# Kernel tuning notes

Hardware: AMD Instinct MI355X
Metric: run time of the kernel (lower is better)

The kernel has to match this reference:

```python
import jax, jax.numpy as jnp
import numpy as np

OVERFLOW_MARGIN = 1e-08
N, BBN_DIM, CBN_DIM = 8192, 32, 512


def setup_inputs() -> dict:
    key = jax.random.key(0)
    k1, k2, k3 = jax.random.split(key, 3)
    bbn = jax.random.uniform(k1, (N, BBN_DIM), dtype=jnp.float32)
    cbn = jax.random.normal(k2, (N, CBN_DIM), dtype=jnp.float32)
    # Dense(cbn_dim) params: glorot-ish init
    W = jax.random.normal(k3, (CBN_DIM, CBN_DIM), dtype=jnp.float32) / np.sqrt(CBN_DIM)
    b = jnp.zeros((CBN_DIM,), dtype=jnp.float32)
    return {"bbn": bbn, "cbn": cbn, "W": W, "b": b}


def reference(bbn, cbn, W, b):
    # --- build_adjacency_hamming(bbn): soft hamming-similarity adjacency [N,N] ---
    code_length = jnp.asarray(bbn.shape[1], dtype=bbn.dtype)
    m1 = bbn - 1.0
    c1 = bbn @ m1.T          # [N,N]
    c2 = m1 @ bbn.T          # [N,N]
    normalized_dist = jnp.abs(c1 + c2) / code_length
    adj = jnp.power(1.0 - normalized_dist, 1.4)

    # --- graph laplacian: D^{-1/2} A D^{-1/2} (broadcast form of eye*d_inv_sqrt matmuls) ---
    d = jnp.sum(adj, axis=1)                      # row sums == adj @ ones
    d_inv_sqrt = jnp.power(d + OVERFLOW_MARGIN, -0.5)
    laplacian = d_inv_sqrt[:, None] * adj * d_inv_sqrt[None, :]

    # --- GCN spectral conv: L @ Dense(cbn), then sigmoid ---
    fc_sc = cbn @ W + b                           # [N, cbn_dim]
    conv_sc = laplacian @ fc_sc                   # [N, cbn_dim]
    return jax.nn.sigmoid(conv_sc)
```

## Files before the change

### kernel.cpp

```cpp
#include <hip/hip_runtime.h>

#define NROWS 8192
#define BBND  32
#define CBND  512
#define JQ    4096
#define NR    64
#define ABUFB 8192

typedef unsigned short u16;
typedef unsigned int   u32;
typedef __bf16 bf16x8 __attribute__((ext_vector_type(8)));
typedef float  f32x4  __attribute__((ext_vector_type(4)));
typedef float  f32x16 __attribute__((ext_vector_type(16)));
typedef u32    u32x4  __attribute__((ext_vector_type(4)));
typedef u32    u32x2  __attribute__((ext_vector_type(2)));

#define ZERO4  (f32x4){0.f,0.f,0.f,0.f}
#define ZERO16 (f32x16){0.f,0.f,0.f,0.f,0.f,0.f,0.f,0.f,0.f,0.f,0.f,0.f,0.f,0.f,0.f,0.f}

#define BAR asm volatile("s_waitcnt lgkmcnt(0)\n\ts_barrier" ::: "memory")

static __device__ inline u16 f2bf(float f) {
    unsigned u = __builtin_bit_cast(unsigned, f);
    unsigned r = (u + 0x7FFFu + ((u >> 16) & 1u)) >> 16;
    return (u16)r;
}

static __device__ inline float pow14(float base) {
    return __builtin_amdgcn_exp2f(1.4f * __builtin_amdgcn_logf(base));
}

static __device__ inline float adj_eval(float dot, float sij) {
    float x = fabsf(2.f * dot - sij);
    float base = fmaxf(1.f - x * (1.f / 32.f), 0.f);
    return pow14(base);
}

static __device__ inline float sigmoidf_fast(float v) {
    float e = __builtin_amdgcn_exp2f(-1.44269504f * v);
    return 1.f / (1.f + e);
}

static __device__ inline u32 cvtpk(float a, float b) {
    u32 r;
    asm("v_cvt_pk_bf16_f32 %0, %1, %2" : "=v"(r) : "v"(a), "v"(b));
    return r;
}

static __device__ inline f32x4 MFMA16(bf16x8 a, bf16x8 b, f32x4 c) {
    return __builtin_amdgcn_mfma_f32_16x16x32_bf16(a, b, c, 0, 0, 0);
}
static __device__ inline f32x16 MFMA32(bf16x8 a, bf16x8 b, f32x16 c) {
    return __builtin_amdgcn_mfma_f32_32x32x16_bf16(a, b, c, 0, 0, 0);
}

__global__ __launch_bounds__(256) void k_prep_rows(const float* __restrict__ bbn,
                                                   float* __restrict__ s,
                                                   u16* __restrict__ bbn_bf) {
    int i = blockIdx.x * 256 + threadIdx.x;
    if (i >= NROWS) return;
    const f32x4* row = reinterpret_cast<const f32x4*>(bbn + i * BBND);
    float sum = 0.f;
    u16* dst = bbn_bf + i * BBND;
#pragma unroll
    for (int q = 0; q < 8; ++q) {
        f32x4 v = row[q];
#pragma unroll
        for (int e = 0; e < 4; ++e) {
            sum += v[e];
            dst[q * 4 + e] = f2bf(v[e]);
        }
    }
    s[i] = sum;
}

__global__ __launch_bounds__(256) void k_prep_wt(const float* __restrict__ W,
                                                 u16* __restrict__ WT) {
    int idx = blockIdx.x * 256 + threadIdx.x;
    int c = idx >> 9, k = idx & 511;
    WT[idx] = f2bf(W[k * CBND + c]);
}

__global__ __launch_bounds__(1024) void k_deg(const u16* __restrict__ bbn_bf,
                                              const float* __restrict__ s,
                                              float* __restrict__ dinv) {
    __shared__ float part[16][16];
    int ibase = blockIdx.x * 16;
    int tid = threadIdx.x;
    int w = tid >> 6, l = tid & 63, lg = l >> 4, lr = l & 15;

    bf16x8 afrag = *reinterpret_cast<const bf16x8*>(bbn_bf + (ibase + lr) * BBND + lg * 8);
    float si[4];
#pragma unroll
    for (int r = 0; r < 4; ++r) si[r] = s[ibase + lg * 4 + r];

    float dacc[4] = {0.f, 0.f, 0.f, 0.f};
    int j0 = w * (NROWS / 16);
    bf16x8 nbf = *reinterpret_cast<const bf16x8*>(bbn_bf + (j0 + lr) * BBND + lg * 8);
    float nsj = s[j0 + lr];
    for (int jt = 0; jt < NROWS / 16; jt += 16) {
        bf16x8 bfrag = nbf;
        float sj = nsj;
        if (jt + 16 < NROWS / 16) {
            int jn = j0 + jt + 16;
            nbf = *reinterpret_cast<const bf16x8*>(bbn_bf + (jn + lr) * BBND + lg * 8);
            nsj = s[jn + lr];
        }
        f32x4 dot = MFMA16(afrag, bfrag, ZERO4);
#pragma unroll
        for (int r = 0; r < 4; ++r) dacc[r] += adj_eval(dot[r], si[r] + sj);
    }
#pragma unroll
    for (int off = 1; off < 16; off <<= 1)
#pragma unroll
        for (int r = 0; r < 4; ++r) dacc[r] += __shfl_xor(dacc[r], off, 64);

    if (lr == 0) {
#pragma unroll
        for (int r = 0; r < 4; ++r) part[w][lg * 4 + r] = dacc[r];
    }
    __syncthreads();
    if (tid < 16) {
        float d = 0.f;
#pragma unroll
        for (int q = 0; q < 16; ++q) d += part[q][tid];
        dinv[ibase + tid] = rsqrtf(d + 1e-8f);
    }
}

__global__ __launch_bounds__(512) void k_fc(const float* __restrict__ cbn,
                                            const u16* __restrict__ WT,
                                            const float* __restrict__ bvec,
                                            const float* __restrict__ dinv,
                                            u16* __restrict__ g_blk) {
    __shared__ __align__(16) u16 Clds[64 * 512];
    int bx = blockIdx.x;
    int ch = bx & 1;
    int jcol = (bx >> 1) * 64;
    int tid = threadIdx.x;
    int w = tid >> 6, l = tid & 63, lg = l >> 4, lr = l & 15;
    int wq = w & 3, jh = w >> 2;

    char* Cl = (char*)&Clds[0];

#pragma unroll
    for (int p = 0; p < 8; ++p) {
        int gidx = p * 512 + tid;
        int row = gidx >> 6, sl = gidx & 63;
        const f32x4* src = reinterpret_cast<const f32x4*>(cbn + (jcol + row) * CBND + sl * 8);
        f32x4 v0 = src[0], v1 = src[1];
        bf16x8 bv;
#pragma unroll
        for (int e = 0; e < 4; ++e) { bv[e] = (__bf16)v0[e]; bv[e + 4] = (__bf16)v1[e]; }
        *reinterpret_cast<bf16x8*>(Cl + row * 1024 + ((sl ^ (row & 7)) << 4)) = bv;
    }
    __syncthreads();

    int r7 = lr & 7;
    for (int q = 0; q < 4; ++q) {
        int cb = ch * 4 + q;
        int crow = cb * 64 + wq * 16;
        f32x4 acc0 = ZERO4, acc1 = ZERO4;
        for (int k0 = 0; k0 < CBND; k0 += 32) {
            bf16x8 afrag = *reinterpret_cast<const bf16x8*>(WT + (crow + lr) * CBND + k0 + lg * 8);
            int slot = (k0 >> 3) + lg;
            int row0 = jh * 32 + lr;
            bf16x8 b0 = *reinterpret_cast<const bf16x8*>(Cl + row0 * 1024 + ((slot ^ r7) << 4));
            bf16x8 b1 = *reinterpret_cast<const bf16x8*>(Cl + (row0 + 16) * 1024 + ((slot ^ r7) << 4));
            acc0 = MFMA16(afrag, b0, acc0);
            acc1 = MFMA16(afrag, b1, acc1);
        }
#pragma unroll
        for (int f = 0; f < 2; ++f) {
            f32x4 af = f ? acc1 : acc0;
#pragma unroll
            for (int r = 0; r < 4; ++r) {
                int c = crow + lg * 4 + r;
                int j = jcol + jh * 32 + f * 16 + lr;
                float val = af[r] + bvec[c];
                g_blk[(((j >> 3) * 512 + c) << 3) + (j & 7)] = f2bf(val * dinv[j]);
            }
        }
    }
}


#define LOADB(T, R) { \
    const char* p = gB + (long)(T) * 65536; \
    R##0 = *reinterpret_cast<const u32x4*>(p); \
    R##1 = *reinterpret_cast<const u32x4*>(p + 16384); \
    R##2 = *reinterpret_cast<const u32x4*>(p + 32768); \
    R##3 = *reinterpret_cast<const u32x4*>(p + 49152); \
}

#define LOADG(ST) { \
    int jg = jbase + (ST) * 64 + jq8 * 16; \
    gJ = *reinterpret_cast<const bf16x8*>(bbn_bf + (jg + lr) * BBND + lg * 8); \
    gS = *reinterpret_cast<const f32x4*>(s + jg + lg * 4); \
}

#define GENP(WB) { \
    f32x4 dot = MFMA16(gJ, fragI, ZERO4); \
    u32 p0 = cvtpk(adj_eval(dot[0], si + gS[0]), adj_eval(dot[1], si + gS[1])); \
    u32 p1 = cvtpk(adj_eval(dot[2], si + gS[2]), adj_eval(dot[3], si + gS[3])); \
    *reinterpret_cast<u32x2*>(Ab + (WB) * ABUFB + gw) = (u32x2){p0, p1}; \
}

#define CONVP(RB, R) { \
    const char* Ar = Ab + (RB) * ABUFB; \
    bf16x8 t0l = *reinterpret_cast<const bf16x8*>(Ar + a0); \
    bf16x8 t0h = *reinterpret_cast<const bf16x8*>(Ar + a0 + 4096); \
    c00 = MFMA32(t0l, __builtin_bit_cast(bf16x8, R##0), c00); \
    c10 = MFMA32(t0h, __builtin_bit_cast(bf16x8, R##0), c10); \
    bf16x8 t1l = *reinterpret_cast<const bf16x8*>(Ar + a1); \
    bf16x8 t1h = *reinterpret_cast<const bf16x8*>(Ar + a1 + 4096); \
    c00 = MFMA32(t1l, __builtin_bit_cast(bf16x8, R##1), c00); \
    c10 = MFMA32(t1h, __builtin_bit_cast(bf16x8, R##1), c10); \
    bf16x8 t2l = *reinterpret_cast<const bf16x8*>(Ar + a2); \
    bf16x8 t2h = *reinterpret_cast<const bf16x8*>(Ar + a2 + 4096); \
    c00 = MFMA32(t2l, __builtin_bit_cast(bf16x8, R##2), c00); \
    c10 = MFMA32(t2h, __builtin_bit_cast(bf16x8, R##2), c10); \
    bf16x8 t3l = *reinterpret_cast<const bf16x8*>(Ar + a3); \
    bf16x8 t3h = *reinterpret_cast<const bf16x8*>(Ar + a3 + 4096); \
    c00 = MFMA32(t3l, __builtin_bit_cast(bf16x8, R##3), c00); \
    c10 = MFMA32(t3h, __builtin_bit_cast(bf16x8, R##3), c10); \
}

#define EPI(ACC, IH) { \
    _Pragma("unroll") \
    for (int reg = 0; reg < 16; ++reg) { \
        int rowD = (reg & 3) + 8 * (reg >> 2) + 4 * lh; \
        Pq[(long)(ibase + (IH) * 32 + rowD) * CBND + w * 32 + l31] = ACC[reg]; \
    } \
}

__global__ __launch_bounds__(1024, 4) void k_conv(const u16* __restrict__ bbn_bf,
                                                  const float* __restrict__ s,
                                                  const u16* __restrict__ g_blk,
                                                  float* __restrict__ P) {
    __shared__ __align__(16) u16 Alds[2][64 * 64];

    int bx = blockIdx.x;
    int jq = bx & 1;
    int it = bx >> 1;
    int ibase = it * 64;
    int jbase = jq * JQ;

    int tid = threadIdx.x;
    int w = tid >> 6, l = tid & 63;
    int lr = l & 15, lg = l >> 4, l31 = l & 31, lh = l >> 5;
    int iq = w & 3, jq8 = w >> 2;

    bf16x8 fragI = *reinterpret_cast<const bf16x8*>(bbn_bf + (ibase + iq * 16 + lr) * BBND + lg * 8);
    float si = s[ibase + iq * 16 + lr];

    char* Ab = (char*)&Alds[0][0];
    float* Pq = P + (long)jq * (NROWS * CBND);

    const char* gB = (const char*)g_blk + (long)jbase * 1024 + lh * 8192
                   + (w * 32 + l31) * 16;

    int r7 = l31 & 7;
    int abase = l31 * 128;
    int a0 = abase + (((0 + lh) ^ r7) << 4);
    int a1 = abase + (((2 + lh) ^ r7) << 4);
    int a2 = abase + (((4 + lh) ^ r7) << 4);
    int a3 = abase + (((6 + lh) ^ r7) << 4);

    int grow = iq * 16 + lr;
    int gw = grow * 128 + (((jq8 * 2 + (lg >> 1)) ^ (grow & 7)) << 4) + (lg & 1) * 8;

    f32x16 c00 = ZERO16, c10 = ZERO16;

    u32x4 rA0, rA1, rA2, rA3;
    u32x4 rB0, rB1, rB2, rB3;
    bf16x8 gJ;
    f32x4 gS;

    LOADG(0);
    GENP(0);
    LOADG(1);
    LOADB(0, rA);
    BAR;

    for (int st2 = 0; st2 < NR; st2 += 2) {
        LOADB(st2 + 1, rB);
        GENP(1);
        if (st2 + 2 < NR) LOADG(st2 + 2);
        CONVP(0, rA);
        BAR;
        int tn = (st2 + 2 < NR) ? st2 + 2 : NR - 1;
        LOADB(tn, rA);
        if (st2 + 2 < NR) {
            GENP(0);
            if (st2 + 3 < NR) LOADG(st2 + 3);
        }
        CONVP(1, rB);
        BAR;
    }

    EPI(c00, 0);
    EPI(c10, 1);
}

__global__ __launch_bounds__(256) void k_comb(const float* __restrict__ dinv,
                                              const float* __restrict__ P,
                                              float* __restrict__ out) {
    int idx = blockIdx.x * 256 + threadIdx.x;
    float di = dinv[idx >> 7];
    f32x4 a = *reinterpret_cast<const f32x4*>(P + (long)idx * 4);
    f32x4 b = *reinterpret_cast<const f32x4*>(P + (long)NROWS * CBND + (long)idx * 4);
    f32x4 v;
#pragma unroll
    for (int e = 0; e < 4; ++e) v[e] = sigmoidf_fast((a[e] + b[e]) * di);
    *reinterpret_cast<f32x4*>(out + (long)idx * 4) = v;
}

extern "C" void kernel_launch(void* const* d_in, const int* in_sizes, int n_in,
                              void* d_out, int out_size, void* d_ws, size_t ws_size,
                              hipStream_t stream) {
    const float* bbn = (const float*)d_in[0];
    const float* cbn = (const float*)d_in[1];
    const float* W   = (const float*)d_in[2];
    const float* b   = (const float*)d_in[3];
    float* out = (float*)d_out;

    char* ws = (char*)d_ws;
    float* s      = (float*)ws;  ws += NROWS * 4;
    float* dinv   = (float*)ws;  ws += NROWS * 4;
    u16* bbn_bf   = (u16*)ws;    ws += NROWS * BBND * 2;
    u16* WT       = (u16*)ws;    ws += CBND * CBND * 2;
    u16* g_blk    = (u16*)ws;    ws += (size_t)CBND * NROWS * 2;
    float* P      = (float*)ws;  ws += (size_t)2 * NROWS * CBND * 4;

    k_prep_rows<<<NROWS / 256, 256, 0, stream>>>(bbn, s, bbn_bf);
    k_prep_wt<<<(CBND * CBND) / 256, 256, 0, stream>>>(W, WT);
    k_deg<<<NROWS / 16, 1024, 0, stream>>>(bbn_bf, s, dinv);
    k_fc<<<(NROWS / 64) * 2, 512, 0, stream>>>(cbn, WT, b, dinv, g_blk);
    k_conv<<<(NROWS / 64) * 2, 1024, 0, stream>>>(bbn_bf, s, g_blk, P);
    k_comb<<<(NROWS * CBND / 4) / 256, 256, 0, stream>>>(dinv, P, out);
}
```

Baseline: 148.7 us.

## Fuse all six stages into one cooperative persistent kernel with grid syncs

Merges row prep, weight transpose, degree computation, the dense layer, the graph convolution and the sigmoid combine into a single kernel launched cooperatively with 256 blocks of 1024 threads. Stages are separated by grid-wide barriers, and one shared-memory buffer is reused across them. This targets the launch gaps and tail idle time between the six small kernels. The cost is that the early stages run with far fewer threads and a different work split, and every grid sync adds its own latency. The 64 KB of shared memory per block may also limit occupancy.

Result: slower. 265.8 us (+78.8%).

```diff
diff --git a/kernel.cpp b/kernel.cpp
--- a/kernel.cpp
+++ b/kernel.cpp
@@ -1,4 +1,7 @@
 #include <hip/hip_runtime.h>
+#include <hip/hip_cooperative_groups.h>
+
+namespace cg = cooperative_groups;
 
 #define NROWS 8192
 #define BBND  32
@@ -53,137 +56,6 @@
 static __device__ inline f32x16 MFMA32(bf16x8 a, bf16x8 b, f32x16 c) {
     return __builtin_amdgcn_mfma_f32_32x32x16_bf16(a, b, c, 0, 0, 0);
 }
-
-__global__ __launch_bounds__(256) void k_prep_rows(const float* __restrict__ bbn,
-                                                   float* __restrict__ s,
-                                                   u16* __restrict__ bbn_bf) {
-    int i = blockIdx.x * 256 + threadIdx.x;
-    if (i >= NROWS) return;
-    const f32x4* row = reinterpret_cast<const f32x4*>(bbn + i * BBND);
-    float sum = 0.f;
-    u16* dst = bbn_bf + i * BBND;
-#pragma unroll
-    for (int q = 0; q < 8; ++q) {
-        f32x4 v = row[q];
-#pragma unroll
-        for (int e = 0; e < 4; ++e) {
-            sum += v[e];
-            dst[q * 4 + e] = f2bf(v[e]);
-        }
-    }
-    s[i] = sum;
-}
-
-__global__ __launch_bounds__(256) void k_prep_wt(const float* __restrict__ W,
-                                                 u16* __restrict__ WT) {
-    int idx = blockIdx.x * 256 + threadIdx.x;
-    int c = idx >> 9, k = idx & 511;
-    WT[idx] = f2bf(W[k * CBND + c]);
-}
-
-__global__ __launch_bounds__(1024) void k_deg(const u16* __restrict__ bbn_bf,
-                                              const float* __restrict__ s,
-                                              float* __restrict__ dinv) {
-    __shared__ float part[16][16];
-    int ibase = blockIdx.x * 16;
-    int tid = threadIdx.x;
-    int w = tid >> 6, l = tid & 63, lg = l >> 4, lr = l & 15;
-
-    bf16x8 afrag = *reinterpret_cast<const bf16x8*>(bbn_bf + (ibase + lr) * BBND + lg * 8);
-    float si[4];
-#pragma unroll
-    for (int r = 0; r < 4; ++r) si[r] = s[ibase + lg * 4 + r];
-
-    float dacc[4] = {0.f, 0.f, 0.f, 0.f};
-    int j0 = w * (NROWS / 16);
-    bf16x8 nbf = *reinterpret_cast<const bf16x8*>(bbn_bf + (j0 + lr) * BBND + lg * 8);
-    float nsj = s[j0 + lr];
-    for (int jt = 0; jt < NROWS / 16; jt += 16) {
-        bf16x8 bfrag = nbf;
-        float sj = nsj;
-        if (jt + 16 < NROWS / 16) {
-            int jn = j0 + jt + 16;
-            nbf = *reinterpret_cast<const bf16x8*>(bbn_bf + (jn + lr) * BBND + lg * 8);
-            nsj = s[jn + lr];
-        }
-        f32x4 dot = MFMA16(afrag, bfrag, ZERO4);
-#pragma unroll
-        for (int r = 0; r < 4; ++r) dacc[r] += adj_eval(dot[r], si[r] + sj);
-    }
-#pragma unroll
-    for (int off = 1; off < 16; off <<= 1)
-#pragma unroll
-        for (int r = 0; r < 4; ++r) dacc[r] += __shfl_xor(dacc[r], off, 64);
-
-    if (lr == 0) {
-#pragma unroll
-        for (int r = 0; r < 4; ++r) part[w][lg * 4 + r] = dacc[r];
-    }
-    __syncthreads();
-    if (tid < 16) {
-        float d = 0.f;
-#pragma unroll
-        for (int q = 0; q < 16; ++q) d += part[q][tid];
-        dinv[ibase + tid] = rsqrtf(d + 1e-8f);
-    }
-}
-
-__global__ __launch_bounds__(512) void k_fc(const float* __restrict__ cbn,
-                                            const u16* __restrict__ WT,
-                                            const float* __restrict__ bvec,
-                                            const float* __restrict__ dinv,
-                                            u16* __restrict__ g_blk) {
-    __shared__ __align__(16) u16 Clds[64 * 512];
-    int bx = blockIdx.x;
-    int ch = bx & 1;
-    int jcol = (bx >> 1) * 64;
-    int tid = threadIdx.x;
-    int w = tid >> 6, l = tid & 63, lg = l >> 4, lr = l & 15;
-    int wq = w & 3, jh = w >> 2;
-
-    char* Cl = (char*)&Clds[0];
-
-#pragma unroll
-    for (int p = 0; p < 8; ++p) {
-        int gidx = p * 512 + tid;
-        int row = gidx >> 6, sl = gidx & 63;
-        const f32x4* src = reinterpret_cast<const f32x4*>(cbn + (jcol + row) * CBND + sl * 8);
-        f32x4 v0 = src[0], v1 = src[1];
-        bf16x8 bv;
-#pragma unroll
-        for (int e = 0; e < 4; ++e) { bv[e] = (__bf16)v0[e]; bv[e + 4] = (__bf16)v1[e]; }
-        *reinterpret_cast<bf16x8*>(Cl + row * 1024 + ((sl ^ (row & 7)) << 4)) = bv;
-    }
-    __syncthreads();
-
-    int r7 = lr & 7;
-    for (int q = 0; q < 4; ++q) {
-        int cb = ch * 4 + q;
-        int crow = cb * 64 + wq * 16;
-        f32x4 acc0 = ZERO4, acc1 = ZERO4;
-        for (int k0 = 0; k0 < CBND; k0 += 32) {
-            bf16x8 afrag = *reinterpret_cast<const bf16x8*>(WT + (crow + lr) * CBND + k0 + lg * 8);
-            int slot = (k0 >> 3) + lg;
-            int row0 = jh * 32 + lr;
-            bf16x8 b0 = *reinterpret_cast<const bf16x8*>(Cl + row0 * 1024 + ((slot ^ r7) << 4));
-            bf16x8 b1 = *reinterpret_cast<const bf16x8*>(Cl + (row0 + 16) * 1024 + ((slot ^ r7) << 4));
-            acc0 = MFMA16(afrag, b0, acc0);
-            acc1 = MFMA16(afrag, b1, acc1);
-        }
-#pragma unroll
-        for (int f = 0; f < 2; ++f) {
-            f32x4 af = f ? acc1 : acc0;
-#pragma unroll
-            for (int r = 0; r < 4; ++r) {
-                int c = crow + lg * 4 + r;
-                int j = jcol + jh * 32 + f * 16 + lr;
-                float val = af[r] + bvec[c];
-                g_blk[(((j >> 3) * 512 + c) << 3) + (j & 7)] = f2bf(val * dinv[j]);
-            }
-        }
-    }
-}
-
 
 #define LOADB(T, R) { \
     const char* p = gB + (long)(T) * 65536; \
@@ -234,86 +106,210 @@
     } \
 }
 
-__global__ __launch_bounds__(1024, 4) void k_conv(const u16* __restrict__ bbn_bf,
-                                                  const float* __restrict__ s,
-                                                  const u16* __restrict__ g_blk,
-                                                  float* __restrict__ P) {
-    __shared__ __align__(16) u16 Alds[2][64 * 64];
+__global__ __launch_bounds__(1024, 4) void k_fused(
+        const float* __restrict__ bbn, const float* __restrict__ cbn,
+        const float* __restrict__ W, const float* __restrict__ bvec,
+        float* __restrict__ out,
+        float* __restrict__ s, float* __restrict__ dinv,
+        u16* __restrict__ bbn_bf, u16* __restrict__ WT,
+        u16* __restrict__ g_blk, float* __restrict__ P) {
+    __shared__ __align__(16) char smem[65536];
+    __shared__ float part[2][8][16];
+
+    cg::grid_group gg = cg::this_grid();
 
     int bx = blockIdx.x;
-    int jq = bx & 1;
-    int it = bx >> 1;
-    int ibase = it * 64;
-    int jbase = jq * JQ;
-
     int tid = threadIdx.x;
     int w = tid >> 6, l = tid & 63;
     int lr = l & 15, lg = l >> 4, l31 = l & 31, lh = l >> 5;
-    int iq = w & 3, jq8 = w >> 2;
-
-    bf16x8 fragI = *reinterpret_cast<const bf16x8*>(bbn_bf + (ibase + iq * 16 + lr) * BBND + lg * 8);
-    float si = s[ibase + iq * 16 + lr];
-
-    char* Ab = (char*)&Alds[0][0];
-    float* Pq = P + (long)jq * (NROWS * CBND);
-
-    const char* gB = (const char*)g_blk + (long)jbase * 1024 + lh * 8192
-                   + (w * 32 + l31) * 16;
-
-    int r7 = l31 & 7;
-    int abase = l31 * 128;
-    int a0 = abase + (((0 + lh) ^ r7) << 4);
-    int a1 = abase + (((2 + lh) ^ r7) << 4);
-    int a2 = abase + (((4 + lh) ^ r7) << 4);
-    int a3 = abase + (((6 + lh) ^ r7) << 4);
-
-    int grow = iq * 16 + lr;
-    int gw = grow * 128 + (((jq8 * 2 + (lg >> 1)) ^ (grow & 7)) << 4) + (lg & 1) * 8;
-
-    f32x16 c00 = ZERO16, c10 = ZERO16;
-
-    u32x4 rA0, rA1, rA2, rA3;
-    u32x4 rB0, rB1, rB2, rB3;
-    bf16x8 gJ;
-    f32x4 gS;
-
-    LOADG(0);
-    GENP(0);
-    LOADG(1);
-    LOADB(0, rA);
-    BAR;
-
-    for (int st2 = 0; st2 < NR; st2 += 2) {
-        LOADB(st2 + 1, rB);
-        GENP(1);
-        if (st2 + 2 < NR) LOADG(st2 + 2);
-        CONVP(0, rA);
+
+    {
+        int idx = bx * 1024 + tid;
+        int c = idx >> 9, k = idx & 511;
+        WT[idx] = f2bf(W[k * CBND + c]);
+        if (idx < NROWS) {
+            const f32x4* row = reinterpret_cast<const f32x4*>(bbn + idx * BBND);
+            float sum = 0.f;
+            u16* dst = bbn_bf + idx * BBND;
+#pragma unroll
+            for (int q = 0; q < 8; ++q) {
+                f32x4 v = row[q];
+#pragma unroll
+                for (int e = 0; e < 4; ++e) {
+                    sum += v[e];
+                    dst[q * 4 + e] = f2bf(v[e]);
+                }
+            }
+            s[idx] = sum;
+        }
+    }
+    gg.sync();
+
+    {
+        int ibase = bx * 32;
+        int ig = w >> 3, jr = w & 7;
+        int ib = ibase + ig * 16;
+        bf16x8 afrag = *reinterpret_cast<const bf16x8*>(bbn_bf + (ib + lr) * BBND + lg * 8);
+        float si[4];
+#pragma unroll
+        for (int r = 0; r < 4; ++r) si[r] = s[ib + lg * 4 + r];
+
+        float dacc[4] = {0.f, 0.f, 0.f, 0.f};
+        int j0 = jr * 1024;
+        bf16x8 nbf = *reinterpret_cast<const bf16x8*>(bbn_bf + (j0 + lr) * BBND + lg * 8);
+        float nsj = s[j0 + lr];
+        for (int jt = 0; jt < 1024; jt += 16) {
+            bf16x8 bfrag = nbf;
+            float sj = nsj;
+            if (jt + 16 < 1024) {
+                int jn = j0 + jt + 16;
+                nbf = *reinterpret_cast<const bf16x8*>(bbn_bf + (jn + lr) * BBND + lg * 8);
+                nsj = s[jn + lr];
+            }
+            f32x4 dot = MFMA16(afrag, bfrag, ZERO4);
+#pragma unroll
+            for (int r = 0; r < 4; ++r) dacc[r] += adj_eval(dot[r], si[r] + sj);
+        }
+#pragma unroll
+        for (int off = 1; off < 16; off <<= 1)
+#pragma unroll
+            for (int r = 0; r < 4; ++r) dacc[r] += __shfl_xor(dacc[r], off, 64);
+
+        if (lr == 0) {
+#pragma unroll
+            for (int r = 0; r < 4; ++r) part[ig][jr][lg * 4 + r] = dacc[r];
+        }
+        __syncthreads();
+        if (tid < 32) {
+            int g2 = tid >> 4, rr = tid & 15;
+            float d = 0.f;
+#pragma unroll
+            for (int q = 0; q < 8; ++q) d += part[g2][q][rr];
+            dinv[ibase + g2 * 16 + rr] = rsqrtf(d + 1e-8f);
+        }
+    }
+    gg.sync();
+
+    {
+        char* Cl = smem;
+        int ch = bx & 1;
+        int jcol = (bx >> 1) * 64;
+#pragma unroll
+        for (int p = 0; p < 4; ++p) {
+            int gidx = p * 1024 + tid;
+            int row = gidx >> 6, sl = gidx & 63;
+            const f32x4* src = reinterpret_cast<const f32x4*>(cbn + (jcol + row) * CBND + sl * 8);
+            f32x4 v0 = src[0], v1 = src[1];
+            bf16x8 bv;
+#pragma unroll
+            for (int e = 0; e < 4; ++e) { bv[e] = (__bf16)v0[e]; bv[e + 4] = (__bf16)v1[e]; }
+            *reinterpret_cast<bf16x8*>(Cl + row * 1024 + ((sl ^ (row & 7)) << 4)) = bv;
+        }
+        __syncthreads();
+
+        int wq = w & 3, jh = (w >> 2) & 1, qh = w >> 3;
+        int r7 = lr & 7;
+#pragma unroll
+        for (int qq = 0; qq < 2; ++qq) {
+            int cb = ch * 4 + qh * 2 + qq;
+            int crow = cb * 64 + wq * 16;
+            f32x4 acc0 = ZERO4, acc1 = ZERO4;
+            for (int k0 = 0; k0 < CBND; k0 += 32) {
+                bf16x8 afrag = *reinterpret_cast<const bf16x8*>(WT + (crow + lr) * CBND + k0 + lg * 8);
+                int slot = (k0 >> 3) + lg;
+                int row0 = jh * 32 + lr;
+                bf16x8 b0 = *reinterpret_cast<const bf16x8*>(Cl + row0 * 1024 + ((slot ^ r7) << 4));
+                bf16x8 b1 = *reinterpret_cast<const bf16x8*>(Cl + (row0 + 16) * 1024 + ((slot ^ r7) << 4));
+                acc0 = MFMA16(afrag, b0, acc0);
+                acc1 = MFMA16(afrag, b1, acc1);
+            }
+#pragma unroll
+            for (int f = 0; f < 2; ++f) {
+                f32x4 af = f ? acc1 : acc0;
+#pragma unroll
+                for (int r = 0; r < 4; ++r) {
+                    int c = crow + lg * 4 + r;
+                    int j = jcol + jh * 32 + f * 16 + lr;
+                    float val = af[r] + bvec[c];
+                    g_blk[(((j >> 3) * 512 + c) << 3) + (j & 7)] = f2bf(val * dinv[j]);
+                }
+            }
+        }
+    }
+    gg.sync();
+
+    {
+        int jq = bx & 1;
+        int it = bx >> 1;
+        int ibase = it * 64;
+        int jbase = jq * JQ;
+        int iq = w & 3, jq8 = w >> 2;
+
+        bf16x8 fragI = *reinterpret_cast<const bf16x8*>(bbn_bf + (ibase + iq * 16 + lr) * BBND + lg * 8);
+        float si = s[ibase + iq * 16 + lr];
+
+        char* Ab = smem;
+        float* Pq = P + (long)jq * (NROWS * CBND);
+
+        const char* gB = (const char*)g_blk + (long)jbase * 1024 + lh * 8192
+                       + (w * 32 + l31) * 16;
+
+        int r7 = l31 & 7;
+        int abase = l31 * 128;
+        int a0 = abase + (((0 + lh) ^ r7) << 4);
+        int a1 = abase + (((2 + lh) ^ r7) << 4);
+        int a2 = abase + (((4 + lh) ^ r7) << 4);
+        int a3 = abase + (((6 + lh) ^ r7) << 4);
+
+        int grow = iq * 16 + lr;
+        int gw = grow * 128 + (((jq8 * 2 + (lg >> 1)) ^ (grow & 7)) << 4) + (lg & 1) * 8;
+
+        f32x16 c00 = ZERO16, c10 = ZERO16;
+        u32x4 rA0, rA1, rA2, rA3;
+        u32x4 rB0, rB1, rB2, rB3;
+        bf16x8 gJ;
+        f32x4 gS;
+
+        LOADG(0);
+        GENP(0);
+        LOADG(1);
+        LOADB(0, rA);
         BAR;
-        int tn = (st2 + 2 < NR) ? st2 + 2 : NR - 1;
-        LOADB(tn, rA);
-        if (st2 + 2 < NR) {
-            GENP(0);
-            if (st2 + 3 < NR) LOADG(st2 + 3);
-        }
-        CONVP(1, rB);
-        BAR;
-    }
-
-    EPI(c00, 0);
-    EPI(c10, 1);
-}
-
-__global__ __launch_bounds__(256) void k_comb(const float* __restrict__ dinv,
-                                              const float* __restrict__ P,
-                                              float* __restrict__ out) {
-    int idx = blockIdx.x * 256 + threadIdx.x;
-    float di = dinv[idx >> 7];
-    f32x4 a = *reinterpret_cast<const f32x4*>(P + (long)idx * 4);
-    f32x4 b = *reinterpret_cast<const f32x4*>(P + (long)NROWS * CBND + (long)idx * 4);
-    f32x4 v;
-#pragma unroll
-    for (int e = 0; e < 4; ++e) v[e] = sigmoidf_fast((a[e] + b[e]) * di);
-    *reinterpret_cast<f32x4*>(out + (long)idx * 4) = v;
+
+        for (int st2 = 0; st2 < NR; st2 += 2) {
+            LOADB(st2 + 1, rB);
+            GENP(1);
+            if (st2 + 2 < NR) LOADG(st2 + 2);
+            CONVP(0, rA);
+            BAR;
+            int tn = (st2 + 2 < NR) ? st2 + 2 : NR - 1;
+            LOADB(tn, rA);
+            if (st2 + 2 < NR) {
+                GENP(0);
+                if (st2 + 3 < NR) LOADG(st2 + 3);
+            }
+            CONVP(1, rB);
+            BAR;
+        }
+
+        EPI(c00, 0);
+        EPI(c10, 1);
+    }
+    gg.sync();
+
+    {
+#pragma unroll
+        for (int t = 0; t < 4; ++t) {
+            int idx = t * 262144 + bx * 1024 + tid;
+            float di = dinv[idx >> 7];
+            f32x4 a = *reinterpret_cast<const f32x4*>(P + (long)idx * 4);
+            f32x4 b = *reinterpret_cast<const f32x4*>(P + (long)NROWS * CBND + (long)idx * 4);
+            f32x4 v;
+#pragma unroll
+            for (int e = 0; e < 4; ++e) v[e] = sigmoidf_fast((a[e] + b[e]) * di);
+            *reinterpret_cast<f32x4*>(out + (long)idx * 4) = v;
+        }
+    }
 }
 
 extern "C" void kernel_launch(void* const* d_in, const int* in_sizes, int n_in,
@@ -333,10 +329,9 @@
     u16* g_blk    = (u16*)ws;    ws += (size_t)CBND * NROWS * 2;
     float* P      = (float*)ws;  ws += (size_t)2 * NROWS * CBND * 4;
 
-    k_prep_rows<<<NROWS / 256, 256, 0, stream>>>(bbn, s, bbn_bf);
-    k_prep_wt<<<(CBND * CBND) / 256, 256, 0, stream>>>(W, WT);
-    k_deg<<<NROWS / 16, 1024, 0, stream>>>(bbn_bf, s, dinv);
-    k_fc<<<(NROWS / 64) * 2, 512, 0, stream>>>(cbn, WT, b, dinv, g_blk);
-    k_conv<<<(NROWS / 64) * 2, 1024, 0, stream>>>(bbn_bf, s, g_blk, P);
-    k_comb<<<(NROWS * CBND / 4) / 256, 256, 0, stream>>>(dinv, P, out);
-}
+    void* kargs[] = {(void*)&bbn, (void*)&cbn, (void*)&W, (void*)&b, (void*)&out,
+                     (void*)&s, (void*)&dinv, (void*)&bbn_bf, (void*)&WT,
+                     (void*)&g_blk, (void*)&P};
+    hipLaunchCooperativeKernel(reinterpret_cast<const void*>(k_fused),
+                               dim3(256), dim3(1024), kargs, 0, stream);
+}
```

## Fuse prep kernels and fold final combine into conv via last-block flag

Applied to the files above, without the earlier changes.

Merges the two prep kernels into one launch that also zeroes a per-row-tile counter array. The separate combine kernel is removed: each conv block atomically increments a counter for its row tile, and the second block to finish sums both partial P halves, scales by dinv and applies the sigmoid. This removes two kernel launches and their gaps, and reads P while it is likely still in cache. In exchange it adds atomics and threadfences, and the tail of the conv kernel becomes uneven because only half the blocks run the epilogue.

Measured after the change: 290.6 us. +95.4%, slower.

```diff
diff --git a/kernel.cpp b/kernel.cpp
--- a/kernel.cpp
+++ b/kernel.cpp
@@ -54,31 +54,31 @@
     return __builtin_amdgcn_mfma_f32_32x32x16_bf16(a, b, c, 0, 0, 0);
 }
 
-__global__ __launch_bounds__(256) void k_prep_rows(const float* __restrict__ bbn,
-                                                   float* __restrict__ s,
-                                                   u16* __restrict__ bbn_bf) {
-    int i = blockIdx.x * 256 + threadIdx.x;
-    if (i >= NROWS) return;
-    const f32x4* row = reinterpret_cast<const f32x4*>(bbn + i * BBND);
-    float sum = 0.f;
-    u16* dst = bbn_bf + i * BBND;
-#pragma unroll
-    for (int q = 0; q < 8; ++q) {
-        f32x4 v = row[q];
-#pragma unroll
-        for (int e = 0; e < 4; ++e) {
-            sum += v[e];
-            dst[q * 4 + e] = f2bf(v[e]);
-        }
-    }
-    s[i] = sum;
-}
-
-__global__ __launch_bounds__(256) void k_prep_wt(const float* __restrict__ W,
-                                                 u16* __restrict__ WT) {
-    int idx = blockIdx.x * 256 + threadIdx.x;
+__global__ __launch_bounds__(512) void k_prep(const float* __restrict__ bbn,
+                                              const float* __restrict__ W,
+                                              float* __restrict__ s,
+                                              u16* __restrict__ bbn_bf,
+                                              u16* __restrict__ WT,
+                                              int* __restrict__ flags) {
+    int idx = blockIdx.x * 512 + threadIdx.x;
     int c = idx >> 9, k = idx & 511;
     WT[idx] = f2bf(W[k * CBND + c]);
+    if (idx < 128) flags[idx] = 0;
+    if (idx < NROWS) {
+        const f32x4* row = reinterpret_cast<const f32x4*>(bbn + idx * BBND);
+        float sum = 0.f;
+        u16* dst = bbn_bf + idx * BBND;
+#pragma unroll
+        for (int q = 0; q < 8; ++q) {
+            f32x4 v = row[q];
+#pragma unroll
+            for (int e = 0; e < 4; ++e) {
+                sum += v[e];
+                dst[q * 4 + e] = f2bf(v[e]);
+            }
+        }
+        s[idx] = sum;
+    }
 }
 
 __global__ __launch_bounds__(1024) void k_deg(const u16* __restrict__ bbn_bf,
@@ -236,9 +236,13 @@
 
 __global__ __launch_bounds__(1024, 4) void k_conv(const u16* __restrict__ bbn_bf,
                                                   const float* __restrict__ s,
+                                                  const float* __restrict__ dinv,
                                                   const u16* __restrict__ g_blk,
-                                                  float* __restrict__ P) {
+                                                  float* __restrict__ P,
+                                                  int* __restrict__ flags,
+                                                  float* __restrict__ out) {
     __shared__ __align__(16) u16 Alds[2][64 * 64];
+    __shared__ int s_old;
 
     int bx = blockIdx.x;
     int jq = bx & 1;
@@ -301,19 +305,27 @@
 
     EPI(c00, 0);
     EPI(c10, 1);
-}
-
-__global__ __launch_bounds__(256) void k_comb(const float* __restrict__ dinv,
-                                              const float* __restrict__ P,
-                                              float* __restrict__ out) {
-    int idx = blockIdx.x * 256 + threadIdx.x;
-    float di = dinv[idx >> 7];
-    f32x4 a = *reinterpret_cast<const f32x4*>(P + (long)idx * 4);
-    f32x4 b = *reinterpret_cast<const f32x4*>(P + (long)NROWS * CBND + (long)idx * 4);
-    f32x4 v;
-#pragma unroll
-    for (int e = 0; e < 4; ++e) v[e] = sigmoidf_fast((a[e] + b[e]) * di);
-    *reinterpret_cast<f32x4*>(out + (long)idx * 4) = v;
+
+    __syncthreads();
+    __threadfence();
+    if (tid == 0) s_old = atomicAdd(&flags[it], 1);
+    __syncthreads();
+    if (s_old == 1) {
+        __threadfence();
+#pragma unroll
+        for (int p = 0; p < 8; ++p) {
+            int idx = p * 1024 + tid;
+            int row = idx >> 7, c4 = idx & 127;
+            long off = (long)(ibase + row) * CBND + c4 * 4;
+            float di = dinv[ibase + row];
+            f32x4 a = *reinterpret_cast<const f32x4*>(P + off);
+            f32x4 b = *reinterpret_cast<const f32x4*>(P + (long)NROWS * CBND + off);
+            f32x4 v;
+#pragma unroll
+            for (int e = 0; e < 4; ++e) v[e] = sigmoidf_fast((a[e] + b[e]) * di);
+            *reinterpret_cast<f32x4*>(out + off) = v;
+        }
+    }
 }
 
 extern "C" void kernel_launch(void* const* d_in, const int* in_sizes, int n_in,
@@ -332,11 +344,10 @@
     u16* WT       = (u16*)ws;    ws += CBND * CBND * 2;
     u16* g_blk    = (u16*)ws;    ws += (size_t)CBND * NROWS * 2;
     float* P      = (float*)ws;  ws += (size_t)2 * NROWS * CBND * 4;
-
-    k_prep_rows<<<NROWS / 256, 256, 0, stream>>>(bbn, s, bbn_bf);
-    k_prep_wt<<<(CBND * CBND) / 256, 256, 0, stream>>>(W, WT);
+    int* flags    = (int*)ws;    ws += 128 * 4;
+
+    k_prep<<<512, 512, 0, stream>>>(bbn, W, s, bbn_bf, WT, flags);
     k_deg<<<NROWS / 16, 1024, 0, stream>>>(bbn_bf, s, dinv);
     k_fc<<<(NROWS / 64) * 2, 512, 0, stream>>>(cbn, WT, b, dinv, g_blk);
-    k_conv<<<(NROWS / 64) * 2, 1024, 0, stream>>>(bbn_bf, s, g_blk, P);
-    k_comb<<<(NROWS * CBND / 4) / 256, 256, 0, stream>>>(dinv, P, out);
-}
+    k_conv<<<(NROWS / 64) * 2, 1024, 0, stream>>>(bbn_bf, s, dinv, g_blk, P, flags, out);
+}
```
